# Kernel tuning notes

Hardware: AMD Instinct MI355X
Metric: run time of the kernel (lower is better)

The kernel has to match this reference:

```python
import jax, jax.numpy as jnp
import numpy as np

# init config (from init_kwargs)
VOXEL_SIZE = np.array([0.25, 0.25, 8.0], dtype=np.float32)
PC_RANGE = np.array([-50.0, -50.0, -5.0, 50.0, 50.0, 3.0], dtype=np.float32)
GRID_SIZE = np.round((PC_RANGE[3:] - PC_RANGE[:3]) / VOXEL_SIZE).astype(np.int64)  # [400, 400, 1]
N_BATCH = 4
N_TIME = 5
N_POINTS = 2_000_000


def setup_inputs() -> dict:
    key = jax.random.key(0)
    kb, kxy, kz, ki, kt = jax.random.split(key, 5)
    # points: [batch_id, x, y, z, intensity, time]; xy generated strictly inside
    # pc_range so the in-range mask in the original forward is all-True (identity
    # filter) -> static shapes, jit-compatible.
    b = jax.random.randint(kb, (N_POINTS, 1), 0, N_BATCH).astype(jnp.float32)
    xy = jax.random.uniform(kxy, (N_POINTS, 2), minval=-49.9, maxval=49.9)
    z = jax.random.uniform(kz, (N_POINTS, 1), minval=-5.0, maxval=3.0)
    inten = jax.random.uniform(ki, (N_POINTS, 1))
    t = jax.random.randint(kt, (N_POINTS, 1), 0, N_TIME).astype(jnp.float32)
    points = jnp.concatenate([b, xy, z, inten, t], axis=1)
    return {"points": points}


def reference(points):
    N = points.shape[0]
    vs = jnp.asarray(VOXEL_SIZE)
    pr = jnp.asarray(PC_RANGE)
    Gx, Gy = int(GRID_SIZE[0]), int(GRID_SIZE[1])

    # voxel coords; all points are in-range by construction (mask identity)
    coords_f = (points[:, 1:4] - pr[:3]) / vs          # (N, 3) float
    coords = coords_f.astype(jnp.int32)                # trunc == floor (coords >= 0)
    b_idx = points[:, 0].astype(jnp.int32)
    t_idx = points[:, -1].astype(jnp.int32)

    # scalar key preserving lexicographic order of (batch, x, y, time)
    key_ = ((b_idx * Gx + coords[:, 0]) * Gy + coords[:, 1]) * N_TIME + t_idx  # (N,)
    unq_keys, unq_inv = jnp.unique(key_, return_inverse=True, size=N, fill_value=-1)

    # scatter_mean of xyz per pillar
    sums = jax.ops.segment_sum(points[:, 1:4], unq_inv, num_segments=N)        # (N, 3)
    cnts = jax.ops.segment_sum(jnp.ones((N,), points.dtype), unq_inv, num_segments=N)
    mean = sums / jnp.maximum(cnts, 1.0)[:, None]

    f_cluster = points[:, 1:4] - mean[unq_inv]
    f_center = points[:, 1:3] - (coords[:, :2].astype(points.dtype) * vs[:2]
                                 + vs[:2] * 0.5 + pr[:2])
    features = jnp.concatenate([points[:, 1:5], f_cluster, f_center], axis=-1)  # (N, 9)

    # decode unique keys back to rows, reordered as (batch, time, y, x);
    # padded slots (key == -1) become -1 rows.
    valid = unq_keys >= 0
    k = jnp.where(valid, unq_keys, 0)
    tt = k % N_TIME
    k = k // N_TIME
    yy = k % Gy
    k = k // Gy
    xx = k % Gx
    bb = k // Gx
    unq = jnp.stack([bb, tt, yy, xx], axis=1)
    unq = jnp.where(valid[:, None], unq, -1)

    return features, unq, unq_inv, jnp.asarray(GRID_SIZE)
```

## Files before the change

kernel.cpp:

```cpp
#include <hip/hip_runtime.h>


#define NKEYS 3200000
#define ELEMS_PER_BLK 1024
#define NBLK (NKEYS / ELEMS_PER_BLK)
#define GX 400
#define GY 400
#define NT 5

__device__ __forceinline__ void accum_point(float b, float x, float y, float z,
                                            float t, unsigned long long* pk) {
    float u = (x + 50.0f) * 4.0f;
    float v = (y + 50.0f) * 4.0f;
    int cx = (int)u;
    int cy = (int)v;
    float dx = u - (float)cx;
    float dy = v - (float)cy;
    float dz = (z + 5.0f) * 0.125f;
    int key = (((int)b * GX + cx) * GY + cy) * NT + (int)t;
    unsigned long long qdx = (unsigned long long)(unsigned int)rintf(dx * 16384.0f);
    unsigned long long qdy = (unsigned long long)(unsigned int)rintf(dy * 16384.0f);
    unsigned long long qdz = (unsigned long long)(unsigned int)rintf(dz * 16384.0f);
    unsigned long long val = qdx | (qdy << 19) | (qdz << 38) | (1ULL << 57);
    atomicAdd(&pk[key], val);
}

__global__ void accum_kernel(const float4* __restrict__ pts4, int npair,
                             unsigned long long* __restrict__ pk) {
    int i = blockIdx.x * blockDim.x + threadIdx.x;
    if (i >= npair) return;
    float4 a = pts4[3 * i + 0];
    float4 b = pts4[3 * i + 1];
    float4 c = pts4[3 * i + 2];
    accum_point(a.x, a.y, a.z, a.w, b.y, pk);
    accum_point(b.z, b.w, c.x, c.y, c.w, pk);
}

__global__ void blocksum_kernel(const unsigned long long* __restrict__ pk,
                                int* __restrict__ bs) {
    __shared__ int red[256];
    int tid = threadIdx.x;
    int base = blockIdx.x * ELEMS_PER_BLK + tid * 4;
    int s = 0;
#pragma unroll
    for (int j = 0; j < 4; ++j) s += (pk[base + j] != 0ULL);
    red[tid] = s;
    __syncthreads();
    for (int off = 128; off > 0; off >>= 1) {
        if (tid < off) red[tid] += red[tid + off];
        __syncthreads();
    }
    if (tid == 0) bs[blockIdx.x] = red[0];
}

__global__ void scan_blocks_kernel(int* __restrict__ bs, int nblk) {
    __shared__ int lds[256];
    int tid = threadIdx.x;
    int carry = 0;
    for (int base = 0; base < nblk; base += 256) {
        int i = base + tid;
        int v = (i < nblk) ? bs[i] : 0;
        lds[tid] = v;
        __syncthreads();
        for (int off = 1; off < 256; off <<= 1) {
            int t = (tid >= off) ? lds[tid - off] : 0;
            __syncthreads();
            lds[tid] += t;
            __syncthreads();
        }
        int incl = lds[tid];
        int total = lds[255];
        __syncthreads();
        if (i < nblk) bs[i] = carry + incl - v;
        carry += total;
    }
    if (tid == 0) bs[nblk] = carry;
}

__global__ void rank_scatter_kernel(unsigned long long* __restrict__ pk,
                                    const int* __restrict__ bs,
                                    float* __restrict__ unq_out) {
    __shared__ int lds[256];
    int tid = threadIdx.x;
    int base = blockIdx.x * ELEMS_PER_BLK + tid * 4;
    unsigned long long c[4];
    int pr[4];
    int s = 0;
#pragma unroll
    for (int j = 0; j < 4; ++j) {
        c[j] = pk[base + j];
        pr[j] = (c[j] != 0ULL);
        s += pr[j];
    }
    lds[tid] = s;
    __syncthreads();
    for (int off = 1; off < 256; off <<= 1) {
        int t = (tid >= off) ? lds[tid - off] : 0;
        __syncthreads();
        lds[tid] += t;
        __syncthreads();
    }
    int run = bs[blockIdx.x] + lds[tid] - s;
#pragma unroll
    for (int j = 0; j < 4; ++j) {
        if (pr[j]) {
            int k = base + j;
            unsigned long long v = c[j];
            float cnt = (float)(unsigned int)(v >> 57);
            float inv = 16383.0f / (16384.0f * cnt);
            unsigned int sx = (unsigned int)(v & 0x7FFFFULL);
            unsigned int sy = (unsigned int)((v >> 19) & 0x7FFFFULL);
            unsigned int sz = (unsigned int)((v >> 38) & 0x7FFFFULL);
            unsigned long long mqx = (unsigned long long)(unsigned int)rintf((float)sx * inv);
            unsigned long long mqy = (unsigned long long)(unsigned int)rintf((float)sy * inv);
            unsigned long long mqz = (unsigned long long)(unsigned int)rintf((float)sz * inv);
            pk[k] = mqx | (mqy << 14) | (mqz << 28) | ((unsigned long long)run << 42);
            int tt = k % NT;
            int k2 = k / NT;
            int yy = k2 % GY;
            int k3 = k2 / GY;
            int xx = k3 % GX;
            int bb = k3 / GX;
            *(float4*)(unq_out + (size_t)run * 4) =
                make_float4((float)bb, (float)tt, (float)yy, (float)xx);
            run++;
        }
    }
}

__global__ void fill_unq_kernel(float4* __restrict__ unq4, int n, float* __restrict__ gs) {
    int i = blockIdx.x * blockDim.x + threadIdx.x;
    if (i == 0) { gs[0] = 400.0f; gs[1] = 400.0f; gs[2] = 1.0f; }
    if (i < n) unq4[i] = make_float4(-1.0f, -1.0f, -1.0f, -1.0f);
}

__device__ __forceinline__ void point_feat(float bfl, float x, float y, float z,
                                           float inten, float t,
                                           const unsigned long long* __restrict__ pk,
                                           float* f, float* r) {
    float u = (x + 50.0f) * 4.0f;
    float v = (y + 50.0f) * 4.0f;
    int cx = (int)u;
    int cy = (int)v;
    int key = (((int)bfl * GX + cx) * GY + cy) * NT + (int)t;
    unsigned long long m = pk[key];
    const float qs = 1.0f / 16383.0f;
    float mdx = (float)(unsigned int)(m & 0x3FFFULL) * qs;
    float mdy = (float)(unsigned int)((m >> 14) & 0x3FFFULL) * qs;
    float mdz = (float)(unsigned int)((m >> 28) & 0x3FFFULL) * qs;
    float bx = (float)cx * 0.25f - 50.0f;
    float by = (float)cy * 0.25f - 50.0f;
    float mx = bx + mdx * 0.25f;
    float my = by + mdy * 0.25f;
    float mz = -5.0f + mdz * 8.0f;
    f[0] = x;
    f[1] = y;
    f[2] = z;
    f[3] = inten;
    f[4] = x - mx;
    f[5] = y - my;
    f[6] = z - mz;
    f[7] = x - (bx + 0.125f);
    f[8] = y - (by + 0.125f);
    *r = (float)(unsigned int)(m >> 42);
}

__global__ void out_kernel(const float4* __restrict__ pts4, int npair,
                           const unsigned long long* __restrict__ pk,
                           float* __restrict__ feat, float2* __restrict__ uinv2) {
    int i = blockIdx.x * blockDim.x + threadIdx.x;
    if (i >= npair) return;
    float4 a = pts4[3 * i + 0];
    float4 b = pts4[3 * i + 1];
    float4 c = pts4[3 * i + 2];
    float f[18];
    float r[2];
    point_feat(a.x, a.y, a.z, a.w, b.x, b.y, pk, f + 0, r + 0);
    point_feat(b.z, b.w, c.x, c.y, c.z, c.w, pk, f + 9, r + 1);
    float2* dst = (float2*)(feat + (size_t)i * 18);
#pragma unroll
    for (int k = 0; k < 9; ++k) dst[k] = make_float2(f[2 * k], f[2 * k + 1]);
    uinv2[i] = make_float2(r[0], r[1]);
}

extern "C" void kernel_launch(void* const* d_in, const int* in_sizes, int n_in,
                              void* d_out, int out_size, void* d_ws, size_t ws_size,
                              hipStream_t stream) {
    const float* pts = (const float*)d_in[0];
    int n = in_sizes[0] / 6;
    int npair = n / 2;

    char* ws = (char*)d_ws;
    unsigned long long* pk = (unsigned long long*)ws;
    int* bs = (int*)(ws + (size_t)NKEYS * 8);

    float* feat = (float*)d_out;
    float* unq  = feat + (size_t)n * 9;
    float* uinv = feat + (size_t)n * 13;
    float* gs   = feat + (size_t)n * 14;

    hipMemsetAsync(pk, 0, (size_t)NKEYS * 8, stream);

    int nb_pts = (n + 255) / 256;
    int nb_pair = (npair + 255) / 256;
    fill_unq_kernel<<<nb_pts, 256, 0, stream>>>((float4*)unq, n, gs);
    accum_kernel<<<nb_pair, 256, 0, stream>>>((const float4*)pts, npair, pk);
    blocksum_kernel<<<NBLK, 256, 0, stream>>>(pk, bs);
    scan_blocks_kernel<<<1, 256, 0, stream>>>(bs, NBLK);
    rank_scatter_kernel<<<NBLK, 256, 0, stream>>>(pk, bs, unq);
    out_kernel<<<nb_pair, 256, 0, stream>>>((const float4*)pts, npair, pk,
                                            feat, (float2*)uinv);
}
```

Baseline: 315.2 us.

## Fuse unq padding fill into output kernel, process four points per thread, wave-scan blocks

Removes the separate fill_unq kernel and instead writes -1 rows only for slots at or beyond the unique count inside the output kernel, which avoids writing the whole unq buffer twice. The accum and output kernels now handle four points per thread with nontemporal 16-byte loads and stores. The single-block scan is replaced by a 1024-thread, shuffle-based scan in one pass, and that kernel also writes the grid size. This cuts launches and redundant memory traffic, at the cost of higher register pressure per thread and a tail path for point counts not divisible by four.

```diff
diff --git a/kernel.cpp b/kernel.cpp
--- a/kernel.cpp
+++ b/kernel.cpp
@@ -7,6 +7,8 @@
 #define GX 400
 #define GY 400
 #define NT 5
+
+typedef __attribute__((ext_vector_type(4))) float vf4;
 
 __device__ __forceinline__ void accum_point(float b, float x, float y, float z,
                                             float t, unsigned long long* pk) {
@@ -21,19 +23,30 @@
     unsigned long long qdx = (unsigned long long)(unsigned int)rintf(dx * 16384.0f);
     unsigned long long qdy = (unsigned long long)(unsigned int)rintf(dy * 16384.0f);
     unsigned long long qdz = (unsigned long long)(unsigned int)rintf(dz * 16384.0f);
-    unsigned long long val = qdx | (qdy << 19) | (qdz << 38) | (1ULL << 57);
-    atomicAdd(&pk[key], val);
-}
-
-__global__ void accum_kernel(const float4* __restrict__ pts4, int npair,
+    atomicAdd(&pk[key], qdx | (qdy << 19) | (qdz << 38) | (1ULL << 57));
+}
+
+__global__ void accum_kernel(const vf4* __restrict__ pts4, int n,
                              unsigned long long* __restrict__ pk) {
     int i = blockIdx.x * blockDim.x + threadIdx.x;
-    if (i >= npair) return;
-    float4 a = pts4[3 * i + 0];
-    float4 b = pts4[3 * i + 1];
-    float4 c = pts4[3 * i + 2];
-    accum_point(a.x, a.y, a.z, a.w, b.y, pk);
-    accum_point(b.z, b.w, c.x, c.y, c.w, pk);
+    int p0 = i * 4;
+    if (p0 + 3 < n) {
+        vf4 a0 = __builtin_nontemporal_load(pts4 + (size_t)6 * i + 0);
+        vf4 a1 = __builtin_nontemporal_load(pts4 + (size_t)6 * i + 1);
+        vf4 a2 = __builtin_nontemporal_load(pts4 + (size_t)6 * i + 2);
+        vf4 a3 = __builtin_nontemporal_load(pts4 + (size_t)6 * i + 3);
+        vf4 a4 = __builtin_nontemporal_load(pts4 + (size_t)6 * i + 4);
+        vf4 a5 = __builtin_nontemporal_load(pts4 + (size_t)6 * i + 5);
+        accum_point(a0.x, a0.y, a0.z, a0.w, a1.y, pk);
+        accum_point(a1.z, a1.w, a2.x, a2.y, a2.w, pk);
+        accum_point(a3.x, a3.y, a3.z, a3.w, a4.y, pk);
+        accum_point(a4.z, a4.w, a5.x, a5.y, a5.w, pk);
+    } else {
+        const float* p = (const float*)pts4;
+        for (int j = p0; j < n; ++j)
+            accum_point(p[6 * j], p[6 * j + 1], p[6 * j + 2], p[6 * j + 3],
+                        p[6 * j + 5], pk);
+    }
 }
 
 __global__ void blocksum_kernel(const unsigned long long* __restrict__ pk,
@@ -53,28 +66,45 @@
     if (tid == 0) bs[blockIdx.x] = red[0];
 }
 
-__global__ void scan_blocks_kernel(int* __restrict__ bs, int nblk) {
-    __shared__ int lds[256];
+__global__ void scan_blocks_kernel(int* __restrict__ bs, float* __restrict__ gs) {
+    __shared__ int wsum[16];
     int tid = threadIdx.x;
-    int carry = 0;
-    for (int base = 0; base < nblk; base += 256) {
-        int i = base + tid;
-        int v = (i < nblk) ? bs[i] : 0;
-        lds[tid] = v;
-        __syncthreads();
-        for (int off = 1; off < 256; off <<= 1) {
-            int t = (tid >= off) ? lds[tid - off] : 0;
-            __syncthreads();
-            lds[tid] += t;
-            __syncthreads();
-        }
-        int incl = lds[tid];
-        int total = lds[255];
-        __syncthreads();
-        if (i < nblk) bs[i] = carry + incl - v;
-        carry += total;
-    }
-    if (tid == 0) bs[nblk] = carry;
+    int lane = tid & 63;
+    int wv = tid >> 6;
+    int j = tid * 4;
+    int v0 = (j + 0 < NBLK) ? bs[j + 0] : 0;
+    int v1 = (j + 1 < NBLK) ? bs[j + 1] : 0;
+    int v2 = (j + 2 < NBLK) ? bs[j + 2] : 0;
+    int v3 = (j + 3 < NBLK) ? bs[j + 3] : 0;
+    int s0 = v0, s1 = s0 + v1, s2 = s1 + v2, s3 = s2 + v3;
+    int x = s3;
+#pragma unroll
+    for (int off = 1; off < 64; off <<= 1) {
+        int y = __shfl_up(x, off, 64);
+        if (lane >= off) x += y;
+    }
+    if (lane == 63) wsum[wv] = x;
+    __syncthreads();
+    if (wv == 0) {
+        int w = (lane < 16) ? wsum[lane] : 0;
+#pragma unroll
+        for (int off = 1; off < 16; off <<= 1) {
+            int y = __shfl_up(w, off, 64);
+            if (lane >= off) w += y;
+        }
+        if (lane < 16) wsum[lane] = w;
+    }
+    __syncthreads();
+    int waveExcl = (wv == 0) ? 0 : wsum[wv - 1];
+    int thrExcl = waveExcl + (x - s3);
+    if (j + 0 < NBLK) bs[j + 0] = thrExcl;
+    if (j + 1 < NBLK) bs[j + 1] = thrExcl + s0;
+    if (j + 2 < NBLK) bs[j + 2] = thrExcl + s1;
+    if (j + 3 < NBLK) bs[j + 3] = thrExcl + s2;
+    if (tid == 0) {
+        bs[NBLK] = wsum[15];
+        gs[0] = 400.0f; gs[1] = 400.0f; gs[2] = 1.0f;
+    }
 }
 
 __global__ void rank_scatter_kernel(unsigned long long* __restrict__ pk,
@@ -121,17 +151,11 @@
             int k3 = k2 / GY;
             int xx = k3 % GX;
             int bb = k3 / GX;
-            *(float4*)(unq_out + (size_t)run * 4) =
-                make_float4((float)bb, (float)tt, (float)yy, (float)xx);
+            vf4 row = {(float)bb, (float)tt, (float)yy, (float)xx};
+            *(vf4*)(unq_out + (size_t)run * 4) = row;
             run++;
         }
     }
-}
-
-__global__ void fill_unq_kernel(float4* __restrict__ unq4, int n, float* __restrict__ gs) {
-    int i = blockIdx.x * blockDim.x + threadIdx.x;
-    if (i == 0) { gs[0] = 400.0f; gs[1] = 400.0f; gs[2] = 1.0f; }
-    if (i < n) unq4[i] = make_float4(-1.0f, -1.0f, -1.0f, -1.0f);
 }
 
 __device__ __forceinline__ void point_feat(float bfl, float x, float y, float z,
@@ -150,37 +174,72 @@
     float mdz = (float)(unsigned int)((m >> 28) & 0x3FFFULL) * qs;
     float bx = (float)cx * 0.25f - 50.0f;
     float by = (float)cy * 0.25f - 50.0f;
-    float mx = bx + mdx * 0.25f;
-    float my = by + mdy * 0.25f;
-    float mz = -5.0f + mdz * 8.0f;
     f[0] = x;
     f[1] = y;
     f[2] = z;
     f[3] = inten;
-    f[4] = x - mx;
-    f[5] = y - my;
-    f[6] = z - mz;
+    f[4] = x - (bx + mdx * 0.25f);
+    f[5] = y - (by + mdy * 0.25f);
+    f[6] = z - (-5.0f + mdz * 8.0f);
     f[7] = x - (bx + 0.125f);
     f[8] = y - (by + 0.125f);
     *r = (float)(unsigned int)(m >> 42);
 }
 
-__global__ void out_kernel(const float4* __restrict__ pts4, int npair,
+__global__ void out_kernel(const vf4* __restrict__ pts4, int n,
                            const unsigned long long* __restrict__ pk,
-                           float* __restrict__ feat, float2* __restrict__ uinv2) {
+                           const int* __restrict__ nu_ptr,
+                           float* __restrict__ feat, vf4* __restrict__ uinv4,
+                           vf4* __restrict__ unq4) {
     int i = blockIdx.x * blockDim.x + threadIdx.x;
-    if (i >= npair) return;
-    float4 a = pts4[3 * i + 0];
-    float4 b = pts4[3 * i + 1];
-    float4 c = pts4[3 * i + 2];
-    float f[18];
-    float r[2];
-    point_feat(a.x, a.y, a.z, a.w, b.x, b.y, pk, f + 0, r + 0);
-    point_feat(b.z, b.w, c.x, c.y, c.z, c.w, pk, f + 9, r + 1);
-    float2* dst = (float2*)(feat + (size_t)i * 18);
-#pragma unroll
-    for (int k = 0; k < 9; ++k) dst[k] = make_float2(f[2 * k], f[2 * k + 1]);
-    uinv2[i] = make_float2(r[0], r[1]);
+    int p0 = i * 4;
+    if (p0 >= n) return;
+    int nu = *nu_ptr;
+    if (p0 + 3 < n) {
+        vf4 a0 = __builtin_nontemporal_load(pts4 + (size_t)6 * i + 0);
+        vf4 a1 = __builtin_nontemporal_load(pts4 + (size_t)6 * i + 1);
+        vf4 a2 = __builtin_nontemporal_load(pts4 + (size_t)6 * i + 2);
+        vf4 a3 = __builtin_nontemporal_load(pts4 + (size_t)6 * i + 3);
+        vf4 a4 = __builtin_nontemporal_load(pts4 + (size_t)6 * i + 4);
+        vf4 a5 = __builtin_nontemporal_load(pts4 + (size_t)6 * i + 5);
+        float f[36];
+        float r[4];
+        point_feat(a0.x, a0.y, a0.z, a0.w, a1.x, a1.y, pk, f + 0, r + 0);
+        point_feat(a1.z, a1.w, a2.x, a2.y, a2.z, a2.w, pk, f + 9, r + 1);
+        point_feat(a3.x, a3.y, a3.z, a3.w, a4.x, a4.y, pk, f + 18, r + 2);
+        point_feat(a4.z, a4.w, a5.x, a5.y, a5.z, a5.w, pk, f + 27, r + 3);
+        vf4* dst = (vf4*)(feat + (size_t)i * 36);
+#pragma unroll
+        for (int k = 0; k < 9; ++k) {
+            vf4 o = {f[4 * k], f[4 * k + 1], f[4 * k + 2], f[4 * k + 3]};
+            __builtin_nontemporal_store(o, dst + k);
+        }
+        vf4 rv = {r[0], r[1], r[2], r[3]};
+        __builtin_nontemporal_store(rv, uinv4 + i);
+#pragma unroll
+        for (int k = 0; k < 4; ++k) {
+            int row = p0 + k;
+            if (row >= nu) {
+                vf4 neg = {-1.0f, -1.0f, -1.0f, -1.0f};
+                unq4[row] = neg;
+            }
+        }
+    } else {
+        const float* p = (const float*)pts4;
+        float* uinv = (float*)uinv4;
+        for (int j = p0; j < n; ++j) {
+            float f[9];
+            float r;
+            point_feat(p[6 * j], p[6 * j + 1], p[6 * j + 2], p[6 * j + 3],
+                       p[6 * j + 4], p[6 * j + 5], pk, f, &r);
+            for (int k = 0; k < 9; ++k) feat[(size_t)j * 9 + k] = f[k];
+            uinv[j] = r;
+            if (j >= nu) {
+                vf4 neg = {-1.0f, -1.0f, -1.0f, -1.0f};
+                unq4[j] = neg;
+            }
+        }
+    }
 }
 
 extern "C" void kernel_launch(void* const* d_in, const int* in_sizes, int n_in,
@@ -188,7 +247,6 @@
                               hipStream_t stream) {
     const float* pts = (const float*)d_in[0];
     int n = in_sizes[0] / 6;
-    int npair = n / 2;
 
     char* ws = (char*)d_ws;
     unsigned long long* pk = (unsigned long long*)ws;
@@ -199,15 +257,14 @@
     float* uinv = feat + (size_t)n * 13;
     float* gs   = feat + (size_t)n * 14;
 
-    hipMemsetAsync(pk, 0, (size_t)NKEYS * 8, stream);
-
-    int nb_pts = (n + 255) / 256;
-    int nb_pair = (npair + 255) / 256;
-    fill_unq_kernel<<<nb_pts, 256, 0, stream>>>((float4*)unq, n, gs);
-    accum_kernel<<<nb_pair, 256, 0, stream>>>((const float4*)pts, npair, pk);
+    (void)hipMemsetAsync(pk, 0, (size_t)NKEYS * 8, stream);
+
+    int nq = (n + 3) / 4;
+    int nb_q = (nq + 255) / 256;
+    accum_kernel<<<nb_q, 256, 0, stream>>>((const vf4*)pts, n, pk);
     blocksum_kernel<<<NBLK, 256, 0, stream>>>(pk, bs);
-    scan_blocks_kernel<<<1, 256, 0, stream>>>(bs, NBLK);
+    scan_blocks_kernel<<<1, 1024, 0, stream>>>(bs, gs);
     rank_scatter_kernel<<<NBLK, 256, 0, stream>>>(pk, bs, unq);
-    out_kernel<<<nb_pair, 256, 0, stream>>>((const float4*)pts, npair, pk,
-                                            feat, (float2*)uinv);
-}
+    out_kernel<<<nb_q, 256, 0, stream>>>((const vf4*)pts, n, pk, bs + NBLK,
+                                         feat, (vf4*)uinv, (vf4*)unq);
+}
```

Measured after the change: 408.6 us. +29.6%, slower.
